# Optimization experiments

Measured on AMD Instinct MI355X. Metric: run time of the kernel, lower is better.

## Reference

```python
import jax, jax.numpy as jnp
import numpy as np

N_NODES = 100000
N_EDGES = 1_600_000
IN_C, HID_C, CLS_C = 128, 256, 64


def setup_inputs() -> dict:
    key = jax.random.key(0)
    ks = jax.random.split(key, 8)
    x = jax.random.normal(ks[0], (N_NODES, IN_C), dtype=jnp.float32)
    edge_index = jax.random.randint(ks[1], (2, N_EDGES), 0, N_NODES, dtype=jnp.int64)
    s1 = 1.0 / np.sqrt(IN_C)
    s2 = 1.0 / np.sqrt(HID_C)
    W1l = jax.random.uniform(ks[2], (IN_C, HID_C), jnp.float32, -s1, s1)
    W1r = jax.random.uniform(ks[3], (IN_C, HID_C), jnp.float32, -s1, s1)
    b1 = jnp.zeros((HID_C,), jnp.float32)
    W2l = jax.random.uniform(ks[4], (HID_C, CLS_C), jnp.float32, -s2, s2)
    W2r = jax.random.uniform(ks[5], (HID_C, CLS_C), jnp.float32, -s2, s2)
    b2 = jnp.zeros((CLS_C,), jnp.float32)
    return {"x": x, "edge_index": edge_index,
            "W1l": W1l, "W1r": W1r, "b1": b1,
            "W2l": W2l, "W2r": W2r, "b2": b2}


def _sage_conv(x, src, dst, Wl, Wr, b, num_nodes):
    # mean aggregation of source features onto destination nodes
    agg = jax.ops.segment_sum(x[src], dst, num_segments=num_nodes)  # [N, F]
    deg = jax.ops.segment_sum(jnp.ones((src.shape[0], 1), x.dtype), dst,
                              num_segments=num_nodes)               # [N, 1]
    agg = agg / jnp.maximum(deg, 1.0)  # zero-degree nodes -> 0
    return agg @ Wl + x @ Wr + b


def reference(x, edge_index, W1l, W1r, b1, W2l, W2r, b2):
    src, dst = edge_index[0], edge_index[1]
    n = x.shape[0]
    h = jax.nn.relu(_sage_conv(x, src, dst, W1l, W1r, b1, n))
    # dropout(p=0.5) is identity in eval mode
    out = _sage_conv(h, src, dst, W2l, W2r, b2, n)
    return jax.nn.sigmoid(out)
```

## Files before the change

kernel.cpp:

```cpp
#include <hip/hip_runtime.h>

typedef __attribute__((ext_vector_type(8))) short short8;
typedef __attribute__((ext_vector_type(4))) float floatx4;
typedef __attribute__((ext_vector_type(2))) float floatx2;

static __device__ __forceinline__ unsigned short f2bf(float f) {
  unsigned int u = __builtin_bit_cast(unsigned int, f);
  u += 0x7FFFu + ((u >> 16) & 1u);
  return (unsigned short)(u >> 16);
}
static __device__ __forceinline__ float bf2f(unsigned short s) {
  unsigned int u = ((unsigned int)s) << 16;
  return __builtin_bit_cast(float, u);
}
static __device__ __forceinline__ unsigned int pk4_fp8(float a, float b, float c, float d) {
  int lo = __builtin_amdgcn_cvt_pk_fp8_f32(a, b, 0, false);
  int hi = __builtin_amdgcn_cvt_pk_fp8_f32(c, d, 0, false);
  return (unsigned int)((lo & 0xffff) | ((hi & 0xffff) << 16));
}
static __device__ __forceinline__ floatx4 unpk4_fp8(unsigned int p) {
  floatx2 lo = __builtin_amdgcn_cvt_pk_f32_fp8((int)p, false);
  floatx2 hi = __builtin_amdgcn_cvt_pk_f32_fp8((int)p, true);
  floatx4 r = {lo.x, lo.y, hi.x, hi.y};
  return r;
}

#define NBUCK 2048
#define BIN_CHUNK 4096
#define SCAP 1536

__global__ __launch_bounds__(256) void binscatter(const int* __restrict__ src,
                                                  const int* __restrict__ dst,
                                                  int* __restrict__ bcnt,
                                                  unsigned int* __restrict__ staging,
                                                  int E) {
  __shared__ int h[NBUCK];
  __shared__ int lstart[NBUCK];
  __shared__ int lcur[NBUCK];
  __shared__ int gbase[NBUCK];
  __shared__ int ps[256];
  __shared__ unsigned int sorted[BIN_CHUNK];
  __shared__ unsigned short bkt[BIN_CHUNK];
  const int t = threadIdx.x;
  for (int i = t; i < NBUCK; i += 256) h[i] = 0;
  __syncthreads();
  const int base = blockIdx.x * BIN_CHUNK;
  int end = base + BIN_CHUNK; if (end > E) end = E;
  const int n = end - base;
  for (int i = base + t; i < end; i += 256)
    atomicAdd(&h[dst[i] >> 6], 1);
  __syncthreads();
  int v[8]; int tsum = 0;
#pragma unroll
  for (int j = 0; j < 8; j++) { v[j] = h[t * 8 + j]; tsum += v[j]; }
  ps[t] = tsum;
  __syncthreads();
  for (int off = 1; off < 256; off <<= 1) {
    int xx = (t >= off) ? ps[t - off] : 0;
    __syncthreads();
    ps[t] += xx;
    __syncthreads();
  }
  int run = ps[t] - tsum;
#pragma unroll
  for (int j = 0; j < 8; j++) {
    lstart[t * 8 + j] = run; lcur[t * 8 + j] = run; run += v[j];
  }
  __syncthreads();
  for (int i = t; i < NBUCK; i += 256)
    gbase[i] = h[i] ? atomicAdd(&bcnt[i], h[i]) : 0;
  for (int i = base + t; i < end; i += 256) {
    int d = dst[i], s = src[i];
    int b = d >> 6;
    int p = atomicAdd(&lcur[b], 1);
    sorted[p] = ((unsigned int)(d & 63) << 17) | (unsigned int)s;
    bkt[p] = (unsigned short)b;
  }
  __syncthreads();
  for (int p = t; p < n; p += 256) {
    int b = bkt[p];
    int g = gbase[b] + (p - lstart[b]);
    if (g < SCAP) staging[(size_t)b * SCAP + g] = sorted[p];
  }
}

__global__ void convxw(const float* __restrict__ x, unsigned int* __restrict__ xq,
                       unsigned short* __restrict__ xbf,
                       const float* __restrict__ W1l, const float* __restrict__ W1r,
                       const float* __restrict__ W2l, const float* __restrict__ W2r,
                       unsigned short* __restrict__ W1p, unsigned short* __restrict__ W2p,
                       int n_nodes) {
  int gi = blockIdx.x * blockDim.x + threadIdx.x;
  const int xwork = n_nodes * 32;
  if (gi < xwork) {
    int node = gi >> 5, c4 = (gi & 31) * 4;
    float4 v = *reinterpret_cast<const float4*>(x + (size_t)node * 128 + c4);
    xq[gi] = pk4_fp8(v.x, v.y, v.z, v.w);
    unsigned short r[4] = { f2bf(v.x), f2bf(v.y), f2bf(v.z), f2bf(v.w) };
    *reinterpret_cast<uint2*>(xbf + (size_t)node * 128 + c4) =
        *reinterpret_cast<uint2*>(r);
    return;
  }
  int i = gi - xwork;
  if (i < 8192) {
    int lane = i & 63, ni = (i >> 6) & 1, kk = (i >> 7) & 7, w = i >> 10;
    int fm = lane & 15, fq = lane >> 4;
    int n = w * 32 + ni * 16 + fm;
    int k0 = kk * 32 + fq * 8;
    unsigned short r[8];
#pragma unroll
    for (int j = 0; j < 8; j++) {
      int k = k0 + j;
      float v = (k < 128) ? W1l[k * 256 + n] : W1r[(k - 128) * 256 + n];
      r[j] = f2bf(v);
    }
    *reinterpret_cast<uint4*>(W1p + (size_t)i * 8) = *reinterpret_cast<uint4*>(r);
  } else if (i < 8192 + 4096) {
    int j2 = i - 8192;
    int lane = j2 & 63, kk = (j2 >> 6) & 7, w = j2 >> 9;
    int fm = lane & 15, fq = lane >> 4;
    int n = w * 16 + fm;
    int k0 = kk * 32 + fq * 8;
    unsigned short r[8];
#pragma unroll
    for (int j = 0; j < 8; j++) {
      int k = k0 + j;
      float v = (n < 64) ? W2l[k * 64 + n] : W2r[k * 64 + (n - 64)];
      r[j] = f2bf(v);
    }
    *reinterpret_cast<uint4*>(W2p + (size_t)j2 * 8) = *reinterpret_cast<uint4*>(r);
  }
}

#define LDSW 264
__global__ __launch_bounds__(512, 6) void gemm_fused(const unsigned short* __restrict__ xbf,
                                                     const uint4* __restrict__ xq,
                                                     const unsigned int* __restrict__ staging,
                                                     const int* __restrict__ bcnt,
                                                     const unsigned short* __restrict__ W1p,
                                                     const unsigned short* __restrict__ W2p,
                                                     const float* __restrict__ b1,
                                                     unsigned char* __restrict__ zq,
                                                     unsigned short* __restrict__ rb,
                                                     int M) {
  __shared__ unsigned short smem[64 * LDSW];
  __shared__ int eidx[SCAP];
  __shared__ int h64[64], rstart[64], cur64[64];
  const int tid = threadIdx.x;
  const int lane = tid & 63;
  const int wave = tid >> 6;
  const int m0 = blockIdx.x * 64;
  const int fm = lane & 15;
  const int fq = lane >> 4;
  const int base = blockIdx.x * SCAP;
  int cnt = bcnt[blockIdx.x]; if (cnt > SCAP) cnt = SCAP;
  const short8* __restrict__ W1v = reinterpret_cast<const short8*>(W1p);
  const short8* __restrict__ W2v = reinterpret_cast<const short8*>(W2p);

  if (tid < 64) h64[tid] = 0;
  __syncthreads();

  unsigned int ew0 = 0, ew1 = 0, ew2 = 0;
  const int i0 = tid, i1 = tid + 512, i2 = tid + 1024;
  if (i0 < cnt) ew0 = staging[base + i0];
  if (i1 < cnt) ew1 = staging[base + i1];
  if (i2 < cnt) ew2 = staging[base + i2];

#pragma unroll
  for (int j = 0; j < 2; j++) {
    int c = j * 512 + tid;
    int row = c >> 4, u4 = c & 15;
    int gr = m0 + row; if (gr >= M) gr = M - 1;
    uint4 v = *reinterpret_cast<const uint4*>(xbf + (size_t)gr * 128 + u4 * 8);
    *reinterpret_cast<uint4*>(&smem[row * LDSW + 128 + u4 * 8]) = v;
  }

  if (i0 < cnt) atomicAdd(&h64[ew0 >> 17], 1);
  if (i1 < cnt) atomicAdd(&h64[ew1 >> 17], 1);
  if (i2 < cnt) atomicAdd(&h64[ew2 >> 17], 1);
  __syncthreads();

  if (tid < 64) {
    int v = h64[tid];
    int s = v;
#pragma unroll
    for (int off = 1; off < 64; off <<= 1) {
      int o = __shfl_up(s, off, 64);
      if (tid >= off) s += o;
    }
    int excl = s - v;
    rstart[tid] = excl;
    cur64[tid] = excl;
  }
  __syncthreads();

  if (i0 < cnt) { int p = atomicAdd(&cur64[ew0 >> 17], 1); eidx[p] = (int)(ew0 & 0x1FFFFu); }
  if (i1 < cnt) { int p = atomicAdd(&cur64[ew1 >> 17], 1); eidx[p] = (int)(ew1 & 0x1FFFFu); }
  if (i2 < cnt) { int p = atomicAdd(&cur64[ew2 >> 17], 1); eidx[p] = (int)(ew2 & 0x1FFFFu); }
  __syncthreads();

  {
    const int grp = lane >> 3;
    const int ch4 = lane & 7;
    int row = wave * 8 + grp;
    int e0l = rstart[row];
    int e1l = e0l + h64[row];
    floatx4 a0[4] = {{0,0,0,0},{0,0,0,0},{0,0,0,0},{0,0,0,0}};
    floatx4 a1[4] = {{0,0,0,0},{0,0,0,0},{0,0,0,0},{0,0,0,0}};
    for (int e = e0l; e < e1l; e += 8) {
      uint4 pb[8];
#pragma unroll
      for (int j = 0; j < 8; j++) {
        int t = e + j; if (t >= e1l) t = e1l - 1;
        int s = eidx[t];
        pb[j] = xq[(s << 3) | ch4];
      }
      int rem = e1l - e;
#pragma unroll
      for (int j = 0; j < 8; j++) {
        if (j < rem) {
          floatx4* acc = (j & 1) ? a1 : a0;
          acc[0] += unpk4_fp8(pb[j].x);
          acc[1] += unpk4_fp8(pb[j].y);
          acc[2] += unpk4_fp8(pb[j].z);
          acc[3] += unpk4_fp8(pb[j].w);
        }
      }
    }
    int d = e1l - e0l; if (d < 1) d = 1;
    float sc = 1.0f / (float)d;
    unsigned short r[16];
#pragma unroll
    for (int j = 0; j < 4; j++) {
      floatx4 a = a0[j] + a1[j];
      r[4 * j + 0] = f2bf(a.x * sc); r[4 * j + 1] = f2bf(a.y * sc);
      r[4 * j + 2] = f2bf(a.z * sc); r[4 * j + 3] = f2bf(a.w * sc);
    }
    unsigned short* dstp = &smem[row * LDSW + ch4 * 16];
    *reinterpret_cast<uint4*>(dstp) = *reinterpret_cast<uint4*>(r);
    *reinterpret_cast<uint4*>(dstp + 8) = *reinterpret_cast<uint4*>(r + 8);
  }

  float bb[2];
#pragma unroll
  for (int ni = 0; ni < 2; ni++) bb[ni] = b1[wave * 32 + ni * 16 + fm];

  __syncthreads();

  floatx4 acc1[4][2] = {};
#pragma unroll 2
  for (int kk = 0; kk < 8; kk++) {
    short8 af[4], bfr[2];
#pragma unroll
    for (int mi = 0; mi < 4; mi++)
      af[mi] = *reinterpret_cast<const short8*>(
          &smem[(mi * 16 + fm) * LDSW + kk * 32 + fq * 8]);
#pragma unroll
    for (int ni = 0; ni < 2; ni++)
      bfr[ni] = W1v[((wave * 8 + kk) * 2 + ni) * 64 + lane];
#pragma unroll
    for (int mi = 0; mi < 4; mi++)
#pragma unroll
      for (int ni = 0; ni < 2; ni++)
        acc1[mi][ni] = __builtin_amdgcn_mfma_f32_16x16x32_bf16(af[mi], bfr[ni],
                                                               acc1[mi][ni], 0, 0, 0);
  }

  __syncthreads();

#pragma unroll
  for (int mi = 0; mi < 4; mi++)
#pragma unroll
    for (int ni = 0; ni < 2; ni++)
#pragma unroll
      for (int r = 0; r < 4; r++) {
        float v = acc1[mi][ni][r] + bb[ni];
        v = v > 0.f ? v : 0.f;
        smem[(mi * 16 + fq * 4 + r) * LDSW + wave * 32 + ni * 16 + fm] = f2bf(v);
      }
  __syncthreads();

  floatx4 acc2[4] = {};
#pragma unroll 2
  for (int kk = 0; kk < 8; kk++) {
    short8 hf[4];
#pragma unroll
    for (int mi = 0; mi < 4; mi++)
      hf[mi] = *reinterpret_cast<const short8*>(
          &smem[(mi * 16 + fm) * LDSW + kk * 32 + fq * 8]);
    short8 wf = W2v[(wave * 8 + kk) * 64 + lane];
#pragma unroll
    for (int mi = 0; mi < 4; mi++)
      acc2[mi] = __builtin_amdgcn_mfma_f32_16x16x32_bf16(hf[mi], wf, acc2[mi], 0, 0, 0);
  }

#pragma unroll
  for (int mi = 0; mi < 4; mi++)
#pragma unroll
    for (int r = 0; r < 4; r++) {
      int grow = m0 + mi * 16 + fq * 4 + r;
      if (grow < M) {
        float v = acc2[mi][r];
        if (wave < 4) {
          int col = wave * 16 + fm;
          int b8 = __builtin_amdgcn_cvt_pk_fp8_f32(v, v, 0, false);
          zq[grow * 64 + col] = (unsigned char)(b8 & 0xff);
        } else {
          int col = (wave - 4) * 16 + fm;
          rb[grow * 64 + col] = f2bf(v);
        }
      }
    }
}

__global__ __launch_bounds__(512, 6) void agg2_final(const uint2* __restrict__ zq2,
                                                     const unsigned short* __restrict__ rb,
                                                     const unsigned int* __restrict__ staging,
                                                     const int* __restrict__ bcnt,
                                                     const float* __restrict__ b2,
                                                     float* __restrict__ out, int n_nodes) {
  __shared__ int eidx[SCAP];
  __shared__ int h64[64], rstart[64], cur64[64];
  const int tid = threadIdx.x;
  const int lane = tid & 63;
  const int wave = tid >> 6;
  const int m0 = blockIdx.x * 64;
  const int base = blockIdx.x * SCAP;
  int cnt = bcnt[blockIdx.x]; if (cnt > SCAP) cnt = SCAP;

  if (tid < 64) h64[tid] = 0;
  __syncthreads();

  unsigned int ew0 = 0, ew1 = 0, ew2 = 0;
  const int i0 = tid, i1 = tid + 512, i2 = tid + 1024;
  if (i0 < cnt) ew0 = staging[base + i0];
  if (i1 < cnt) ew1 = staging[base + i1];
  if (i2 < cnt) ew2 = staging[base + i2];
  if (i0 < cnt) atomicAdd(&h64[ew0 >> 17], 1);
  if (i1 < cnt) atomicAdd(&h64[ew1 >> 17], 1);
  if (i2 < cnt) atomicAdd(&h64[ew2 >> 17], 1);
  __syncthreads();

  if (tid < 64) {
    int v = h64[tid];
    int s = v;
#pragma unroll
    for (int off = 1; off < 64; off <<= 1) {
      int o = __shfl_up(s, off, 64);
      if (tid >= off) s += o;
    }
    rstart[tid] = s - v;
    cur64[tid] = s - v;
  }
  __syncthreads();

  if (i0 < cnt) { int p = atomicAdd(&cur64[ew0 >> 17], 1); eidx[p] = (int)(ew0 & 0x1FFFFu); }
  if (i1 < cnt) { int p = atomicAdd(&cur64[ew1 >> 17], 1); eidx[p] = (int)(ew1 & 0x1FFFFu); }
  if (i2 < cnt) { int p = atomicAdd(&cur64[ew2 >> 17], 1); eidx[p] = (int)(ew2 & 0x1FFFFu); }
  __syncthreads();

  const int grp = lane >> 3;
  const int ch = lane & 7;
  int row = wave * 8 + grp;
  int w = m0 + row;
  if (w >= n_nodes) return;
  int e0l = rstart[row];
  int e1l = e0l + h64[row];
  floatx4 a0[2] = {{0,0,0,0},{0,0,0,0}};
  floatx4 a1[2] = {{0,0,0,0},{0,0,0,0}};
  for (int e = e0l; e < e1l; e += 8) {
    uint2 pb[8];
#pragma unroll
    for (int j = 0; j < 8; j++) {
      int t = e + j; if (t >= e1l) t = e1l - 1;
      int s = eidx[t];
      pb[j] = zq2[(s << 3) | ch];
    }
    int rem = e1l - e;
#pragma unroll
    for (int j = 0; j < 8; j++) {
      if (j < rem) {
        floatx4* acc = (j & 1) ? a1 : a0;
        acc[0] += unpk4_fp8(pb[j].x);
        acc[1] += unpk4_fp8(pb[j].y);
      }
    }
  }
  int d = e1l - e0l; if (d < 1) d = 1;
  float sc = 1.0f / (float)d;
  int c0 = ch * 8;
  uint4 rr = *reinterpret_cast<const uint4*>(rb + (size_t)w * 64 + c0);
  float4 bvA = *reinterpret_cast<const float4*>(b2 + c0);
  float4 bvB = *reinterpret_cast<const float4*>(b2 + c0 + 4);
  floatx4 s0 = a0[0] + a1[0];
  floatx4 s1 = a0[1] + a1[1];
  float4 oA, oB;
  oA.x = 1.0f / (1.0f + __expf(-(s0.x * sc + bf2f((unsigned short)(rr.x & 0xffff)) + bvA.x)));
  oA.y = 1.0f / (1.0f + __expf(-(s0.y * sc + bf2f((unsigned short)(rr.x >> 16)) + bvA.y)));
  oA.z = 1.0f / (1.0f + __expf(-(s0.z * sc + bf2f((unsigned short)(rr.y & 0xffff)) + bvA.z)));
  oA.w = 1.0f / (1.0f + __expf(-(s0.w * sc + bf2f((unsigned short)(rr.y >> 16)) + bvA.w)));
  oB.x = 1.0f / (1.0f + __expf(-(s1.x * sc + bf2f((unsigned short)(rr.z & 0xffff)) + bvB.x)));
  oB.y = 1.0f / (1.0f + __expf(-(s1.y * sc + bf2f((unsigned short)(rr.z >> 16)) + bvB.y)));
  oB.z = 1.0f / (1.0f + __expf(-(s1.z * sc + bf2f((unsigned short)(rr.w & 0xffff)) + bvB.z)));
  oB.w = 1.0f / (1.0f + __expf(-(s1.w * sc + bf2f((unsigned short)(rr.w >> 16)) + bvB.w)));
  float* op = out + (size_t)w * 64 + c0;
  *reinterpret_cast<float4*>(op) = oA;
  *reinterpret_cast<float4*>(op + 4) = oB;
}

extern "C" void kernel_launch(void* const* d_in, const int* in_sizes, int n_in,
                              void* d_out, int out_size, void* d_ws, size_t ws_size,
                              hipStream_t stream) {
  const float* x   = (const float*)d_in[0];
  const int*   ei  = (const int*)d_in[1];
  const float* W1l = (const float*)d_in[2];
  const float* W1r = (const float*)d_in[3];
  const float* b1  = (const float*)d_in[4];
  const float* W2l = (const float*)d_in[5];
  const float* W2r = (const float*)d_in[6];
  const float* b2  = (const float*)d_in[7];
  float* out = (float*)d_out;

  const int N = in_sizes[0] / 128;
  const int E = in_sizes[1] / 2;
  const int* src = ei;
  const int* dst = ei + E;

  char* wsb = (char*)d_ws;
  size_t off = 0;
  auto alloc = [&](size_t bytes) -> void* {
    void* p = wsb + off;
    off += (bytes + 511) & ~(size_t)511;
    return p;
  };
  int* bcnt     = (int*)alloc(NBUCK * 4);
  unsigned int* staging = (unsigned int*)alloc((size_t)NBUCK * SCAP * 4);
  unsigned short* W1p = (unsigned short*)alloc(256 * 256 * 2);
  unsigned short* W2p = (unsigned short*)alloc(128 * 256 * 2);
  unsigned int* xq    = (unsigned int*)alloc((size_t)N * 128);
  unsigned short* xbf = (unsigned short*)alloc((size_t)N * 128 * 2);
  unsigned char* zq   = (unsigned char*)alloc((size_t)N * 64);
  unsigned short* rb  = (unsigned short*)alloc((size_t)N * 64 * 2);
  (void)ws_size; (void)n_in; (void)out_size;

  const int ntiles = (N + 63) / 64;
  const int nchunks = (E + BIN_CHUNK - 1) / BIN_CHUNK;
  const int convblocks = (N * 32 + 8192 + 4096 + 255) / 256;

  hipMemsetAsync(bcnt, 0, NBUCK * 4, stream);
  binscatter<<<nchunks, 256, 0, stream>>>(src, dst, bcnt, staging, E);

  convxw<<<convblocks, 256, 0, stream>>>(x, xq, xbf, W1l, W1r, W2l, W2r, W1p, W2p, N);

  gemm_fused<<<ntiles, 512, 0, stream>>>(xbf, (const uint4*)xq, staging, bcnt,
                                         W1p, W2p, b1, zq, rb, N);

  agg2_final<<<ntiles, 512, 0, stream>>>((const uint2*)zq, rb, staging, bcnt,
                                         b2, out, N);
}
```

Before: 217.1 us.

## Merge binscatter and convert kernels, reuse per-tile CSR in second aggregation

Combines the edge-binning kernel and the x/weight conversion kernel into one launch, with blocks chosen by block index, so the two independent preprocessing jobs can overlap and one launch is saved. The first fused GEMM kernel now writes its locally sorted edge indices and per-row start/degree to global memory. The second aggregation kernel reads those directly instead of redoing the histogram, scan and local scatter. Binning also uses less shared memory by folding three arrays into one offset array, which may raise occupancy. The cost is extra global writes and reads for the CSR arrays, and a larger merged kernel whose shared memory footprint also applies to the conversion blocks.

```diff
diff --git a/kernel.cpp b/kernel.cpp
--- a/kernel.cpp
+++ b/kernel.cpp
@@ -29,68 +29,72 @@
 #define BIN_CHUNK 4096
 #define SCAP 1536
 
-__global__ __launch_bounds__(256) void binscatter(const int* __restrict__ src,
-                                                  const int* __restrict__ dst,
-                                                  int* __restrict__ bcnt,
-                                                  unsigned int* __restrict__ staging,
-                                                  int E) {
+__global__ __launch_bounds__(256) void prep(const int* __restrict__ src,
+                                            const int* __restrict__ dst,
+                                            int* __restrict__ bcnt,
+                                            unsigned int* __restrict__ staging,
+                                            int E, int nchunks,
+                                            const float* __restrict__ x,
+                                            unsigned int* __restrict__ xq,
+                                            unsigned short* __restrict__ xbf,
+                                            const float* __restrict__ W1l,
+                                            const float* __restrict__ W1r,
+                                            const float* __restrict__ W2l,
+                                            const float* __restrict__ W2r,
+                                            unsigned short* __restrict__ W1p,
+                                            unsigned short* __restrict__ W2p,
+                                            int n_nodes) {
   __shared__ int h[NBUCK];
-  __shared__ int lstart[NBUCK];
-  __shared__ int lcur[NBUCK];
-  __shared__ int gbase[NBUCK];
+  __shared__ int cur[NBUCK];
   __shared__ int ps[256];
   __shared__ unsigned int sorted[BIN_CHUNK];
   __shared__ unsigned short bkt[BIN_CHUNK];
-  const int t = threadIdx.x;
-  for (int i = t; i < NBUCK; i += 256) h[i] = 0;
-  __syncthreads();
-  const int base = blockIdx.x * BIN_CHUNK;
-  int end = base + BIN_CHUNK; if (end > E) end = E;
-  const int n = end - base;
-  for (int i = base + t; i < end; i += 256)
-    atomicAdd(&h[dst[i] >> 6], 1);
-  __syncthreads();
-  int v[8]; int tsum = 0;
-#pragma unroll
-  for (int j = 0; j < 8; j++) { v[j] = h[t * 8 + j]; tsum += v[j]; }
-  ps[t] = tsum;
-  __syncthreads();
-  for (int off = 1; off < 256; off <<= 1) {
-    int xx = (t >= off) ? ps[t - off] : 0;
-    __syncthreads();
-    ps[t] += xx;
-    __syncthreads();
-  }
-  int run = ps[t] - tsum;
-#pragma unroll
-  for (int j = 0; j < 8; j++) {
-    lstart[t * 8 + j] = run; lcur[t * 8 + j] = run; run += v[j];
-  }
-  __syncthreads();
-  for (int i = t; i < NBUCK; i += 256)
-    gbase[i] = h[i] ? atomicAdd(&bcnt[i], h[i]) : 0;
-  for (int i = base + t; i < end; i += 256) {
-    int d = dst[i], s = src[i];
-    int b = d >> 6;
-    int p = atomicAdd(&lcur[b], 1);
-    sorted[p] = ((unsigned int)(d & 63) << 17) | (unsigned int)s;
-    bkt[p] = (unsigned short)b;
-  }
-  __syncthreads();
-  for (int p = t; p < n; p += 256) {
-    int b = bkt[p];
-    int g = gbase[b] + (p - lstart[b]);
-    if (g < SCAP) staging[(size_t)b * SCAP + g] = sorted[p];
-  }
-}
-
-__global__ void convxw(const float* __restrict__ x, unsigned int* __restrict__ xq,
-                       unsigned short* __restrict__ xbf,
-                       const float* __restrict__ W1l, const float* __restrict__ W1r,
-                       const float* __restrict__ W2l, const float* __restrict__ W2r,
-                       unsigned short* __restrict__ W1p, unsigned short* __restrict__ W2p,
-                       int n_nodes) {
-  int gi = blockIdx.x * blockDim.x + threadIdx.x;
+  if (blockIdx.x < nchunks) {
+    const int t = threadIdx.x;
+    for (int i = t; i < NBUCK; i += 256) h[i] = 0;
+    __syncthreads();
+    const int base = blockIdx.x * BIN_CHUNK;
+    int end = base + BIN_CHUNK; if (end > E) end = E;
+    const int n = end - base;
+    for (int i = base + t; i < end; i += 256)
+      atomicAdd(&h[dst[i] >> 6], 1);
+    __syncthreads();
+    int v[8]; int tsum = 0;
+#pragma unroll
+    for (int j = 0; j < 8; j++) { v[j] = h[t * 8 + j]; tsum += v[j]; }
+    ps[t] = tsum;
+    __syncthreads();
+    for (int off = 1; off < 256; off <<= 1) {
+      int xx = (t >= off) ? ps[t - off] : 0;
+      __syncthreads();
+      ps[t] += xx;
+      __syncthreads();
+    }
+    int run = ps[t] - tsum;
+#pragma unroll
+    for (int j = 0; j < 8; j++) { cur[t * 8 + j] = run; run += v[j]; }
+    __syncthreads();
+    for (int i = t; i < NBUCK; i += 256) {
+      int hv = h[i];
+      h[i] = (hv ? atomicAdd(&bcnt[i], hv) : 0) - cur[i];
+    }
+    __syncthreads();
+    for (int i = base + t; i < end; i += 256) {
+      int d = dst[i], s = src[i];
+      int b = d >> 6;
+      int p = atomicAdd(&cur[b], 1);
+      sorted[p] = ((unsigned int)(d & 63) << 17) | (unsigned int)s;
+      bkt[p] = (unsigned short)b;
+    }
+    __syncthreads();
+    for (int p = t; p < n; p += 256) {
+      int b = bkt[p];
+      int g = p + h[b];
+      if (g < SCAP) staging[(size_t)b * SCAP + g] = sorted[p];
+    }
+    return;
+  }
+  int gi = (blockIdx.x - nchunks) * 256 + threadIdx.x;
   const int xwork = n_nodes * 32;
   if (gi < xwork) {
     int node = gi >> 5, c4 = (gi & 31) * 4;
@@ -142,6 +146,9 @@
                                                      const float* __restrict__ b1,
                                                      unsigned char* __restrict__ zq,
                                                      unsigned short* __restrict__ rb,
+                                                     int* __restrict__ csr,
+                                                     int* __restrict__ rsg,
+                                                     int* __restrict__ degg,
                                                      int M) {
   __shared__ unsigned short smem[64 * LDSW];
   __shared__ int eidx[SCAP];
@@ -199,6 +206,12 @@
   if (i2 < cnt) { int p = atomicAdd(&cur64[ew2 >> 17], 1); eidx[p] = (int)(ew2 & 0x1FFFFu); }
   __syncthreads();
 
+  for (int i = tid; i < cnt; i += 512) csr[base + i] = eidx[i];
+  if (tid < 64) {
+    int w = m0 + tid;
+    if (w < M) { rsg[w] = rstart[tid]; degg[w] = h64[tid]; }
+  }
+
   {
     const int grp = lane >> 3;
     const int ch4 = lane & 7;
@@ -315,12 +328,13 @@
 
 __global__ __launch_bounds__(512, 6) void agg2_final(const uint2* __restrict__ zq2,
                                                      const unsigned short* __restrict__ rb,
-                                                     const unsigned int* __restrict__ staging,
+                                                     const int* __restrict__ csr,
+                                                     const int* __restrict__ rsg,
+                                                     const int* __restrict__ degg,
                                                      const int* __restrict__ bcnt,
                                                      const float* __restrict__ b2,
                                                      float* __restrict__ out, int n_nodes) {
   __shared__ int eidx[SCAP];
-  __shared__ int h64[64], rstart[64], cur64[64];
   const int tid = threadIdx.x;
   const int lane = tid & 63;
   const int wave = tid >> 6;
@@ -328,35 +342,7 @@
   const int base = blockIdx.x * SCAP;
   int cnt = bcnt[blockIdx.x]; if (cnt > SCAP) cnt = SCAP;
 
-  if (tid < 64) h64[tid] = 0;
-  __syncthreads();
-
-  unsigned int ew0 = 0, ew1 = 0, ew2 = 0;
-  const int i0 = tid, i1 = tid + 512, i2 = tid + 1024;
-  if (i0 < cnt) ew0 = staging[base + i0];
-  if (i1 < cnt) ew1 = staging[base + i1];
-  if (i2 < cnt) ew2 = staging[base + i2];
-  if (i0 < cnt) atomicAdd(&h64[ew0 >> 17], 1);
-  if (i1 < cnt) atomicAdd(&h64[ew1 >> 17], 1);
-  if (i2 < cnt) atomicAdd(&h64[ew2 >> 17], 1);
-  __syncthreads();
-
-  if (tid < 64) {
-    int v = h64[tid];
-    int s = v;
-#pragma unroll
-    for (int off = 1; off < 64; off <<= 1) {
-      int o = __shfl_up(s, off, 64);
-      if (tid >= off) s += o;
-    }
-    rstart[tid] = s - v;
-    cur64[tid] = s - v;
-  }
-  __syncthreads();
-
-  if (i0 < cnt) { int p = atomicAdd(&cur64[ew0 >> 17], 1); eidx[p] = (int)(ew0 & 0x1FFFFu); }
-  if (i1 < cnt) { int p = atomicAdd(&cur64[ew1 >> 17], 1); eidx[p] = (int)(ew1 & 0x1FFFFu); }
-  if (i2 < cnt) { int p = atomicAdd(&cur64[ew2 >> 17], 1); eidx[p] = (int)(ew2 & 0x1FFFFu); }
+  for (int i = tid; i < cnt; i += 512) eidx[i] = csr[base + i];
   __syncthreads();
 
   const int grp = lane >> 3;
@@ -364,8 +350,9 @@
   int row = wave * 8 + grp;
   int w = m0 + row;
   if (w >= n_nodes) return;
-  int e0l = rstart[row];
-  int e1l = e0l + h64[row];
+  int e0l = rsg[w];
+  int e1l = e0l + degg[w];
+  if (e1l > cnt) e1l = cnt;
   floatx4 a0[2] = {{0,0,0,0},{0,0,0,0}};
   floatx4 a1[2] = {{0,0,0,0},{0,0,0,0}};
   for (int e = e0l; e < e1l; e += 8) {
@@ -435,6 +422,9 @@
   };
   int* bcnt     = (int*)alloc(NBUCK * 4);
   unsigned int* staging = (unsigned int*)alloc((size_t)NBUCK * SCAP * 4);
+  int* csr      = (int*)alloc((size_t)NBUCK * SCAP * 4);
+  int* rsg      = (int*)alloc((size_t)N * 4);
+  int* degg     = (int*)alloc((size_t)N * 4);
   unsigned short* W1p = (unsigned short*)alloc(256 * 256 * 2);
   unsigned short* W2p = (unsigned short*)alloc(128 * 256 * 2);
   unsigned int* xq    = (unsigned int*)alloc((size_t)N * 128);
@@ -448,13 +438,13 @@
   const int convblocks = (N * 32 + 8192 + 4096 + 255) / 256;
 
   hipMemsetAsync(bcnt, 0, NBUCK * 4, stream);
-  binscatter<<<nchunks, 256, 0, stream>>>(src, dst, bcnt, staging, E);
-
-  convxw<<<convblocks, 256, 0, stream>>>(x, xq, xbf, W1l, W1r, W2l, W2r, W1p, W2p, N);
+  prep<<<nchunks + convblocks, 256, 0, stream>>>(src, dst, bcnt, staging, E, nchunks,
+                                                 x, xq, xbf, W1l, W1r, W2l, W2r,
+                                                 W1p, W2p, N);
 
   gemm_fused<<<ntiles, 512, 0, stream>>>(xbf, (const uint4*)xq, staging, bcnt,
-                                         W1p, W2p, b1, zq, rb, N);
-
-  agg2_final<<<ntiles, 512, 0, stream>>>((const uint2*)zq, rb, staging, bcnt,
+                                         W1p, W2p, b1, zq, rb, csr, rsg, degg, N);
+
+  agg2_final<<<ntiles, 512, 0, stream>>>((const uint2*)zq, rb, csr, rsg, degg, bcnt,
                                          b2, out, N);
 }
```

New measurement: 218.4 us. Within noise of the previous version (+0.6%).
